# Performance work log

Measured on AMD Instinct MI355X. Metric: run time of the kernel, lower is better.

## Reference

```python
import jax, jax.numpy as jnp
import numpy as np

EPS = 1e-5
QMAX = 127.0

def setup_inputs() -> dict:
    key = jax.random.key(0)
    k_x, k_w = jax.random.split(key)
    B, S, DIN, DOUT = 8, 2048, 4096, 4096
    x = jax.random.normal(k_x, (B, S, DIN), dtype=jnp.float32)
    # Learned full-precision weight (kaiming-normal, fan_out) then ternarized,
    # mimicking BitLinear._post_init -> terniarize(params).
    std = np.sqrt(2.0 / DOUT)
    w_fp = jax.random.normal(k_w, (DOUT, DIN), dtype=jnp.float32) * std
    scale_w = 1.0 / jnp.clip(jnp.mean(jnp.abs(w_fp)), 1e-5)   # scalar, matches terniarize
    w_ternary = jnp.clip(jnp.round(w_fp * scale_w), -1.0, 1.0)  # values in {-1,0,1}, stored as f32
    gamma = jnp.ones((DIN,), dtype=jnp.float32)                 # RMSNorm weight
    bias = jnp.zeros((DOUT,), dtype=jnp.float32)                # init.constant_(bias, 0)
    return {"x": x, "w_ternary": w_ternary, "scale_w": scale_w, "gamma": gamma, "bias": bias}

def reference(x, w_ternary, scale_w, gamma, bias):
    # 1) RMSNorm over last dim (in_features)
    var = jnp.mean(jnp.square(x), axis=-1, keepdims=True)
    xn = x * jax.lax.rsqrt(var + EPS) * gamma
    # 2) bitmat: per-token absmax int8 quantization of activations
    scale_x = QMAX / jnp.clip(jnp.max(jnp.abs(xn), axis=-1, keepdims=True), 1e-5)  # [B,S,1]
    xq = jnp.clip(jnp.round(xn * scale_x), -128.0, 127.0)
    # 3) ternary matmul (int math expressed in f32) + inline dequant by scale_x*scale_w
    acc = jnp.einsum('bsk,ok->bso', xq, w_ternary)  # [B,S,DOUT]
    out = acc / (scale_x * scale_w)
    # 4) bias
    return out + bias
```

## Files before the change

kernel.cpp:

```cpp
#include <hip/hip_runtime.h>
#include <cstdint>

#define DIN 4096
#define DOUT 4096
#define QMAXF 127.0f

typedef int v4i __attribute__((ext_vector_type(4)));
typedef unsigned int u32;

__device__ __forceinline__ void async16(const void* g, void* l) {
  __builtin_amdgcn_global_load_lds((const __attribute__((address_space(1))) u32*)g,
                                   (__attribute__((address_space(3))) u32*)l,
                                   16, 0, 0);
}

__device__ __forceinline__ int clamp_q(float v) {
  int i = (int)rintf(v);
  return i < -128 ? -128 : (i > 127 ? 127 : i);
}

__global__ __launch_bounds__(256) void wconvert_kernel(const float* __restrict__ w,
                                                       int8_t* __restrict__ wq) {
  int t = blockIdx.x * 256 + threadIdx.x;
  float4 v = ((const float4*)w)[t];
  int b0 = ((int)v.x) & 255, b1 = ((int)v.y) & 255;
  int b2 = ((int)v.z) & 255, b3 = ((int)v.w) & 255;
  ((int*)wq)[t] = b0 | (b1 << 8) | (b2 << 16) | (b3 << 24);
}

__global__ __launch_bounds__(256) void rmsnorm_quant_kernel(
    const float* __restrict__ x, const float* __restrict__ gamma,
    const float* __restrict__ scale_w_ptr, int8_t* __restrict__ xq,
    float* __restrict__ inv_scale) {
  const int token = blockIdx.x;
  const float* xr = x + (size_t)token * DIN;
  const int t = threadIdx.x;

  float4 xv[4], gv[4];
  float ss = 0.f, amax = 0.f;
#pragma unroll
  for (int i = 0; i < 4; ++i) {
    const int idx = (i * 256 + t) * 4;
    xv[i] = *(const float4*)(xr + idx);
    gv[i] = *(const float4*)(gamma + idx);
    ss += xv[i].x * xv[i].x + xv[i].y * xv[i].y + xv[i].z * xv[i].z + xv[i].w * xv[i].w;
    amax = fmaxf(amax, fabsf(xv[i].x * gv[i].x));
    amax = fmaxf(amax, fabsf(xv[i].y * gv[i].y));
    amax = fmaxf(amax, fabsf(xv[i].z * gv[i].z));
    amax = fmaxf(amax, fabsf(xv[i].w * gv[i].w));
  }
#pragma unroll
  for (int o = 32; o > 0; o >>= 1) {
    ss += __shfl_down(ss, o);
    amax = fmaxf(amax, __shfl_down(amax, o));
  }
  __shared__ float s_ss[4], s_am[4];
  const int wave = t >> 6, lane = t & 63;
  if (lane == 0) { s_ss[wave] = ss; s_am[wave] = amax; }
  __syncthreads();
  const float tot = s_ss[0] + s_ss[1] + s_ss[2] + s_ss[3];
  const float mx = fmaxf(fmaxf(s_am[0], s_am[1]), fmaxf(s_am[2], s_am[3]));
  const float rstd = rsqrtf(tot * (1.0f / DIN) + 1e-5f);
  const float absmax = fmaxf(mx * rstd, 1e-5f);
  const float qscale = rstd * (QMAXF / absmax);
  if (t == 0) inv_scale[token] = absmax / (QMAXF * scale_w_ptr[0]);

  int* qr = (int*)(xq + (size_t)token * DIN);
#pragma unroll
  for (int i = 0; i < 4; ++i) {
    const int idx4 = i * 256 + t;
    int b0 = clamp_q(xv[i].x * gv[i].x * qscale) & 255;
    int b1 = clamp_q(xv[i].y * gv[i].y * qscale) & 255;
    int b2 = clamp_q(xv[i].z * gv[i].z * qscale) & 255;
    int b3 = clamp_q(xv[i].w * gv[i].w * qscale) & 255;
    qr[idx4] = b0 | (b1 << 8) | (b2 << 16) | (b3 << 24);
  }
}

#define BM 128
#define BN 128
#define BK 64

__global__ __launch_bounds__(256) void gemm_i8_kernel(
    const int8_t* __restrict__ xq, const int8_t* __restrict__ wq,
    const float* __restrict__ inv_scale, const float* __restrict__ bias,
    float* __restrict__ out) {
  __shared__ int8_t As[BM * BK];
  __shared__ int8_t Bs[BN * BK];

  const int t = threadIdx.x;
  const int wave = t >> 6;
  const int lane = t & 63;
  const int m0 = blockIdx.y * BM;
  const int n0 = blockIdx.x * BN;

  const int fl0 = t * 16;
  const int fl1 = 4096 + t * 16;
  const int r0 = fl0 >> 6, c0 = fl0 & 63;
  const int r1 = fl1 >> 6;

  const int8_t* Ag = xq + (size_t)m0 * DIN;
  const int8_t* Bg = wq + (size_t)n0 * DIN;

  v4i acc[4][4];
#pragma unroll
  for (int mi = 0; mi < 4; ++mi)
#pragma unroll
    for (int ni = 0; ni < 4; ++ni) acc[mi][ni] = (v4i){0, 0, 0, 0};

  const int wm = (wave >> 1) * 64;
  const int wn = (wave & 1) * 64;
  const int fr = lane & 15;
  const int fk = (lane >> 4) * 16;

  for (int k0 = 0; k0 < DIN; k0 += BK) {
    __syncthreads();
    async16(Ag + (size_t)r0 * DIN + k0 + c0, &As[fl0]);
    async16(Ag + (size_t)r1 * DIN + k0 + c0, &As[fl1]);
    async16(Bg + (size_t)r0 * DIN + k0 + c0, &Bs[fl0]);
    async16(Bg + (size_t)r1 * DIN + k0 + c0, &Bs[fl1]);
    __syncthreads();

    v4i a[4], b[4];
#pragma unroll
    for (int i = 0; i < 4; ++i)
      a[i] = *(const v4i*)(&As[(wm + i * 16 + fr) * BK + fk]);
#pragma unroll
    for (int i = 0; i < 4; ++i)
      b[i] = *(const v4i*)(&Bs[(wn + i * 16 + fr) * BK + fk]);
#pragma unroll
    for (int mi = 0; mi < 4; ++mi)
#pragma unroll
      for (int ni = 0; ni < 4; ++ni)
        acc[mi][ni] = __builtin_amdgcn_mfma_i32_16x16x64_i8(a[mi], b[ni], acc[mi][ni], 0, 0, 0);
  }

  const int col = lane & 15;
  const int rb = (lane >> 4) * 4;
#pragma unroll
  for (int mi = 0; mi < 4; ++mi) {
    float sc[4];
#pragma unroll
    for (int r = 0; r < 4; ++r) sc[r] = inv_scale[m0 + wm + mi * 16 + rb + r];
#pragma unroll
    for (int ni = 0; ni < 4; ++ni) {
      const int gc = n0 + wn + ni * 16 + col;
      const float bb = bias[gc];
#pragma unroll
      for (int r = 0; r < 4; ++r) {
        const int gr = m0 + wm + mi * 16 + rb + r;
        out[(size_t)gr * DOUT + gc] = (float)acc[mi][ni][r] * sc[r] + bb;
      }
    }
  }
}

extern "C" void kernel_launch(void* const* d_in, const int* in_sizes, int n_in,
                              void* d_out, int out_size, void* d_ws, size_t ws_size,
                              hipStream_t stream) {
  const float* x       = (const float*)d_in[0];
  const float* w       = (const float*)d_in[1];
  const float* scale_w = (const float*)d_in[2];
  const float* gamma   = (const float*)d_in[3];
  const float* bias    = (const float*)d_in[4];
  float* out = (float*)d_out;
  const int M = in_sizes[0] / DIN;

  int8_t* wq = (int8_t*)d_ws;
  int8_t* xq = wq + (size_t)DOUT * DIN;
  float* inv_scale = (float*)(xq + (size_t)M * DIN);

  hipLaunchKernelGGL(wconvert_kernel, dim3((DOUT * DIN) / (256 * 4)), dim3(256), 0, stream,
                     w, wq);
  hipLaunchKernelGGL(rmsnorm_quant_kernel, dim3(M), dim3(256), 0, stream,
                     x, gamma, scale_w, xq, inv_scale);
  hipLaunchKernelGGL(gemm_i8_kernel, dim3(DOUT / BN, M / BM), dim3(256), 0, stream,
                     xq, wq, inv_scale, bias, out);
}
```

Before: 864.7 us.

## Double GEMM K-tile to 128 and swizzle LDS layout to avoid bank conflicts

The int8 GEMM K tile grows from 64 to 128. Each block now issues twice as many async global-to-LDS loads per stage and runs two MFMA sub-steps between barriers, so there are half as many synchronisation rounds. The 16-byte chunks of each LDS row are rotated by the row index, and reads use matching precomputed offsets, to reduce LDS bank conflicts on the fragment loads. In exchange the kernel uses twice the shared memory (32 KB) and needs more registers for the offset tables, which may lower occupancy.

```diff
diff --git a/kernel.cpp b/kernel.cpp
--- a/kernel.cpp
+++ b/kernel.cpp
@@ -79,7 +79,7 @@
 
 #define BM 128
 #define BN 128
-#define BK 64
+#define BK 128
 
 __global__ __launch_bounds__(256) void gemm_i8_kernel(
     const int8_t* __restrict__ xq, const int8_t* __restrict__ wq,
@@ -94,10 +94,13 @@
   const int m0 = blockIdx.y * BM;
   const int n0 = blockIdx.x * BN;
 
-  const int fl0 = t * 16;
-  const int fl1 = 4096 + t * 16;
-  const int r0 = fl0 >> 6, c0 = fl0 & 63;
-  const int r1 = fl1 >> 6;
+  int srow[4], scol[4];
+#pragma unroll
+  for (int i = 0; i < 4; ++i) {
+    const int p = i * 256 + t;
+    srow[i] = p >> 3;
+    scol[i] = ((p - (p >> 3)) & 7) * 16;
+  }
 
   const int8_t* Ag = xq + (size_t)m0 * DIN;
   const int8_t* Bg = wq + (size_t)n0 * DIN;
@@ -111,28 +114,41 @@
   const int wm = (wave >> 1) * 64;
   const int wn = (wave & 1) * 64;
   const int fr = lane & 15;
-  const int fk = (lane >> 4) * 16;
+  const int q = lane >> 4;
+
+  int offA[2][4], offB[2][4];
+#pragma unroll
+  for (int s = 0; s < 2; ++s)
+#pragma unroll
+    for (int j = 0; j < 4; ++j) {
+      const int sw = ((s * 4 + q + fr) & 7) * 16;
+      offA[s][j] = (wm + j * 16 + fr) * BK + sw;
+      offB[s][j] = (wn + j * 16 + fr) * BK + sw;
+    }
 
   for (int k0 = 0; k0 < DIN; k0 += BK) {
     __syncthreads();
-    async16(Ag + (size_t)r0 * DIN + k0 + c0, &As[fl0]);
-    async16(Ag + (size_t)r1 * DIN + k0 + c0, &As[fl1]);
-    async16(Bg + (size_t)r0 * DIN + k0 + c0, &Bs[fl0]);
-    async16(Bg + (size_t)r1 * DIN + k0 + c0, &Bs[fl1]);
+#pragma unroll
+    for (int i = 0; i < 4; ++i)
+      async16(Ag + (size_t)srow[i] * DIN + k0 + scol[i], &As[i * 4096 + t * 16]);
+#pragma unroll
+    for (int i = 0; i < 4; ++i)
+      async16(Bg + (size_t)srow[i] * DIN + k0 + scol[i], &Bs[i * 4096 + t * 16]);
     __syncthreads();
 
-    v4i a[4], b[4];
 #pragma unroll
-    for (int i = 0; i < 4; ++i)
-      a[i] = *(const v4i*)(&As[(wm + i * 16 + fr) * BK + fk]);
+    for (int s = 0; s < 2; ++s) {
+      v4i a[4], b[4];
 #pragma unroll
-    for (int i = 0; i < 4; ++i)
-      b[i] = *(const v4i*)(&Bs[(wn + i * 16 + fr) * BK + fk]);
+      for (int j = 0; j < 4; ++j) a[j] = *(const v4i*)(&As[offA[s][j]]);
 #pragma unroll
-    for (int mi = 0; mi < 4; ++mi)
+      for (int j = 0; j < 4; ++j) b[j] = *(const v4i*)(&Bs[offB[s][j]]);
 #pragma unroll
-      for (int ni = 0; ni < 4; ++ni)
-        acc[mi][ni] = __builtin_amdgcn_mfma_i32_16x16x64_i8(a[mi], b[ni], acc[mi][ni], 0, 0, 0);
+      for (int mi = 0; mi < 4; ++mi)
+#pragma unroll
+        for (int ni = 0; ni < 4; ++ni)
+          acc[mi][ni] = __builtin_amdgcn_mfma_i32_16x16x64_i8(a[mi], b[ni], acc[mi][ni], 0, 0, 0);
+    }
   }
 
   const int col = lane & 15;
```

New measurement: 830.3 us. 1.04x faster.
